# Optimization experiments

Hardware: AMD Instinct MI355X
Metric: run time of the kernel (lower is better)

The kernel has to match this reference:

```python
import jax, jax.numpy as jnp
import numpy as np

HIDDEN = 2048
HEADS = 16
HEAD_DIM = HIDDEN // HEADS
BATCH = 2
SEQ = 2048


def setup_inputs() -> dict:
    key = jax.random.key(0)
    ks = jax.random.split(key, 9)
    s = 0.02
    return {
        "x": jax.random.normal(ks[0], (BATCH, SEQ, HIDDEN), dtype=jnp.float32),
        "wq": jax.random.normal(ks[1], (HIDDEN, HIDDEN), dtype=jnp.float32) * s,
        "bq": jax.random.normal(ks[2], (HIDDEN,), dtype=jnp.float32) * s,
        "wk": jax.random.normal(ks[3], (HIDDEN, HIDDEN), dtype=jnp.float32) * s,
        "bk": jax.random.normal(ks[4], (HIDDEN,), dtype=jnp.float32) * s,
        "wv": jax.random.normal(ks[5], (HIDDEN, HIDDEN), dtype=jnp.float32) * s,
        "bv": jax.random.normal(ks[6], (HIDDEN,), dtype=jnp.float32) * s,
        "wo": jax.random.normal(ks[7], (HIDDEN, HIDDEN), dtype=jnp.float32) * s,
        "bo": jax.random.normal(ks[8], (HIDDEN,), dtype=jnp.float32) * s,
    }


def reference(x, wq, bq, wk, bk, wv, bv, wo, bo):
    B, S, _ = x.shape
    scale = jnp.sqrt(jnp.float32(HEAD_DIM))
    # torch Linear: y = x @ W.T + b
    def proj(w, b):
        return (x @ w.T + b).reshape(B, S, HEADS, HEAD_DIM).transpose(0, 2, 1, 3)
    q = proj(wq, bq)  # [B,H,S,D]
    k = proj(wk, bk)
    v = proj(wv, bv)
    scores = jnp.einsum("bhqd,bhkd->bhqk", q, k) / scale  # [B,H,S,S]
    probs = jax.nn.softmax(scores, axis=-1)
    ctx = jnp.einsum("bhqk,bhkd->bhqd", probs, v)  # [B,H,S,D]
    ctx = ctx.transpose(0, 2, 1, 3).reshape(B, S, HIDDEN)
    return ctx @ wo.T + bo
```

## Files before the change

kernel.cpp:

```cpp
#include <hip/hip_runtime.h>

typedef unsigned short u16;
typedef unsigned int   u32;
typedef float  f32x4   __attribute__((ext_vector_type(4)));
typedef __bf16 bf16x8  __attribute__((ext_vector_type(8)));
typedef u16    u16x8   __attribute__((ext_vector_type(8)));
typedef u16    u16x4   __attribute__((ext_vector_type(4)));
typedef u32    u32x2   __attribute__((ext_vector_type(2)));
typedef u32    u32x4   __attribute__((ext_vector_type(4)));

#define HIDDEN 2048
#define SEQ    2048
#define NHEADS 16
#define HD     128
#define BATCH  2
#define QSTR   4096

typedef const __attribute__((address_space(3))) u16* lptr;

__device__ __forceinline__ u16 f2bf(float f) {
  u32 u = __builtin_bit_cast(u32, f);
  u += 0x7FFFu + ((u >> 16) & 1u);
  return (u16)(u >> 16);
}
__device__ __forceinline__ u32 pk2(float a, float b) {
  __bf16 x = (__bf16)a, y = (__bf16)b;
  return (u32)__builtin_bit_cast(u16, x) | ((u32)__builtin_bit_cast(u16, y) << 16);
}
__device__ __forceinline__ bf16x8 ld_frag(const u16* p) {
  return __builtin_bit_cast(bf16x8, *(const u32x4*)p);
}
__device__ __forceinline__ void gload_lds16(const u16* g, u16* l) {
  __builtin_amdgcn_global_load_lds((const __attribute__((address_space(1))) u32*)g,
                                   (__attribute__((address_space(3))) u32*)l, 16, 0, 0);
}

#define DSR(dst, base, lit) \
  asm volatile("ds_read_b128 %0, %1 offset:" lit : "=v"(dst) : "v"(base))

#define MFMA16(d, a, b) d = __builtin_amdgcn_mfma_f32_16x16x32_bf16(a, b, d, 0, 0, 0)

__global__ __launch_bounds__(256) void cvt_kernel(const float* __restrict__ src,
                                                  u16* __restrict__ dst, int n4) {
  int stride = gridDim.x * blockDim.x;
  for (int i = blockIdx.x * blockDim.x + threadIdx.x; i < n4; i += stride) {
    f32x4 v = ((const f32x4*)src)[i];
    u16x4 o;
    o[0] = f2bf(v[0]); o[1] = f2bf(v[1]); o[2] = f2bf(v[2]); o[3] = f2bf(v[3]);
    *(u16x4*)(dst + (size_t)i * 4) = o;
  }
}

__global__ __launch_bounds__(256) void cvt4_kernel(
    const float* __restrict__ s0, const float* __restrict__ s1,
    const float* __restrict__ s2, const float* __restrict__ s3,
    u16* __restrict__ o0, u16* __restrict__ o1,
    u16* __restrict__ o2, u16* __restrict__ o3, int n4) {
  const float* src = (blockIdx.y == 0) ? s0 : (blockIdx.y == 1) ? s1 : (blockIdx.y == 2) ? s2 : s3;
  u16* dst = (blockIdx.y == 0) ? o0 : (blockIdx.y == 1) ? o1 : (blockIdx.y == 2) ? o2 : o3;
  int stride = gridDim.x * blockDim.x;
  for (int i = blockIdx.x * blockDim.x + threadIdx.x; i < n4; i += stride) {
    f32x4 v = ((const f32x4*)src)[i];
    u16x4 o;
    o[0] = f2bf(v[0]); o[1] = f2bf(v[1]); o[2] = f2bf(v[2]); o[3] = f2bf(v[3]);
    *(u16x4*)(dst + (size_t)i * 4) = o;
  }
}

__global__ __launch_bounds__(512, 2) void gemm_qkv(
    const u16* __restrict__ A, const u16* __restrict__ Bt,
    const float* __restrict__ bq, const float* __restrict__ bk,
    const float* __restrict__ bv,
    u16* __restrict__ qk, u16* __restrict__ vtb, float qscale)
{
  __shared__ __attribute__((aligned(16))) u16 As[2][16384];
  __shared__ __attribute__((aligned(16))) u16 Bs[2][12288];

  const int tid  = threadIdx.x;
  const int lane = tid & 63;
  const int wave = tid >> 6;
  const int l15  = lane & 15;
  const int g    = lane >> 4;
  const int wm   = wave >> 2;
  const int wn   = wave & 3;

  const int id  = blockIdx.x;
  const int xcd = id & 7;
  const int c   = id >> 3;
  const int tileN = (xcd * 4 + (c >> 4)) * 192;
  const int tileM = (c & 15) << 8;

  const int srow = tid >> 3;
  const int gch8 = ((tid & 7) ^ (srow & 7)) * 8;
  const u16* agp = A  + (size_t)(tileM + srow) * HIDDEN + gch8;
  const u16* bgp = Bt + (size_t)(tileN + srow) * HIDDEN + gch8;
  u16* asp = (u16*)&As[0][0] + tid * 8;
  u16* bsp = (u16*)&Bs[0][0] + tid * 8;

  auto stage = [&](int buf, int ko) {
    u16* ad = asp + buf * 16384;
    u16* bd = bsp + buf * 12288;
#pragma unroll
    for (int r = 0; r < 4; ++r)
      gload_lds16(agp + (size_t)r * 64 * HIDDEN + ko, ad + r * 4096);
#pragma unroll
    for (int r = 0; r < 3; ++r)
      gload_lds16(bgp + (size_t)r * 64 * HIDDEN + ko, bd + r * 4096);
  };

  const int sw = l15 & 7;
  const int c0 = (g ^ sw) * 8;
  const int c1 = ((g ^ sw) ^ 4) * 8;
  lptr aT = (lptr)&As[0][0] + (size_t)(wm * 128 + l15) * 64;
  lptr bT = (lptr)&Bs[0][0] + (size_t)(wn * 48 + l15) * 64;

  f32x4 acc[8][3] = {};
  bf16x8 Xa[8], Xb[3], Ya[8], Yb[3];

#define ISSUE_SET(Sa, Sb, ab, bb)      \
  DSR(Sa[0], ab, "0");                 \
  DSR(Sa[1], ab, "2048");              \
  DSR(Sa[2], ab, "4096");              \
  DSR(Sa[3], ab, "6144");              \
  DSR(Sa[4], ab, "8192");              \
  DSR(Sa[5], ab, "10240");             \
  DSR(Sa[6], ab, "12288");             \
  DSR(Sa[7], ab, "14336");             \
  DSR(Sb[0], bb, "0");                 \
  DSR(Sb[1], bb, "2048");              \
  DSR(Sb[2], bb, "4096");

#define MFMA24(Sa, Sb)                                                                    \
  _Pragma("unroll")                                                                       \
  for (int mf = 0; mf < 8; ++mf) {                                                        \
    _Pragma("unroll")                                                                     \
    for (int nf = 0; nf < 3; ++nf)                                                        \
      acc[mf][nf] = __builtin_amdgcn_mfma_f32_16x16x32_bf16(Sa[mf], Sb[nf], acc[mf][nf], 0, 0, 0); \
  }

  stage(0, 0);
  stage(1, 64);
  asm volatile("s_waitcnt vmcnt(7)" ::: "memory");
  __builtin_amdgcn_s_barrier();
  __builtin_amdgcn_sched_barrier(0);
  {
    lptr ab = aT + c0;
    lptr bb = bT + c0;
    ISSUE_SET(Xa, Xb, ab, bb)
  }

#pragma unroll 2
  for (int t = 0; t < 32; ++t) {
    const int cur = t & 1;
    lptr aC = aT + cur * 16384;
    lptr bC = bT + cur * 12288;
    {
      lptr ab = aC + c1;
      lptr bb = bC + c1;
      ISSUE_SET(Ya, Yb, ab, bb)
    }
    asm volatile("s_waitcnt lgkmcnt(11)" ::: "memory");
    __builtin_amdgcn_sched_barrier(0);
    __builtin_amdgcn_s_setprio(1);
    MFMA24(Xa, Xb)
    __builtin_amdgcn_s_setprio(0);
    asm volatile("s_waitcnt lgkmcnt(0)" ::: "memory");
    __builtin_amdgcn_sched_barrier(0);
    __builtin_amdgcn_s_setprio(1);
    MFMA24(Ya, Yb)
    __builtin_amdgcn_s_setprio(0);
    __builtin_amdgcn_s_barrier();
    __builtin_amdgcn_sched_barrier(0);
    if (t < 30) {
      stage(cur, (t + 2) * 64);
      asm volatile("s_waitcnt vmcnt(7)" ::: "memory");
    } else {
      asm volatile("s_waitcnt vmcnt(0)" ::: "memory");
    }
    __builtin_amdgcn_s_barrier();
    __builtin_amdgcn_sched_barrier(0);
    if (t < 31) {
      lptr ab = aT + (cur ^ 1) * 16384 + c0;
      lptr bb = bT + (cur ^ 1) * 12288 + c0;
      ISSUE_SET(Xa, Xb, ab, bb)
    }
  }

#pragma unroll
  for (int mi = 0; mi < 8; ++mi) {
#pragma unroll
    for (int ni = 0; ni < 3; ++ni) {
      const int gcb = tileN + wn * 48 + ni * 16;
      const int seg = gcb >> 11;
      const int gc  = gcb + l15;
      const float bvv = ((seg == 0) ? bq : (seg == 1) ? bk : bv)[gc & 2047];
      if (seg < 2) {
        const float scl = (seg == 0) ? qscale : 1.f;
#pragma unroll
        for (int j = 0; j < 4; ++j) {
          const int gr = tileM + wm * 128 + mi * 16 + g * 4 + j;
          qk[(size_t)gr * QSTR + gc] = f2bf((acc[mi][ni][j] + bvv) * scl);
        }
      } else {
        const int dglob = gc - 4096;
        const int hh = dglob >> 7, dd = dglob & 127;
        const int srow0 = tileM + wm * 128 + mi * 16 + g * 4;
        const int bb = srow0 >> 11, ss = srow0 & 2047;
        u16x4 o;
#pragma unroll
        for (int j = 0; j < 4; ++j) o[j] = f2bf(acc[mi][ni][j] + bvv);
        *(u16x4*)(vtb + ((size_t)((bb * NHEADS + hh) * HD + dd)) * SEQ + ss) = o;
      }
    }
  }
#undef ISSUE_SET
#undef MFMA24
}

__global__ __launch_bounds__(256, 2) void gemm_bt(
    const u16* __restrict__ A, const u16* __restrict__ Bt,
    const float* __restrict__ bias, float* __restrict__ Cout,
    int M, int N, int K)
{
  __shared__ __attribute__((aligned(16))) u16 As[128 * 32];
  __shared__ __attribute__((aligned(16))) u16 Bs[128 * 32];
  const int tid  = threadIdx.x;
  const int lane = tid & 63;
  const int wave = tid >> 6;

  const int nbx   = N >> 7;
  const int nby   = M >> 7;
  const int id    = blockIdx.x;
  const int xcd   = id & 7;
  const int c     = id >> 3;
  const int cpx   = nbx >> 3;
  const int tileN = (xcd * cpx + c / nby) << 7;
  const int tileM = (c % nby) << 7;

  const int g = lane >> 4, r = lane & 15;

  const int srow = lane >> 2;
  const int scol = (lane & 3) * 8;
  const u16* ag0 = A  + (size_t)(tileM + wave * 16 + srow) * K + scol;
  const u16* ag1 = ag0 + (size_t)64 * K;
  const u16* bg0 = Bt + (size_t)(tileN + wave * 16 + srow) * K + scol;
  const u16* bg1 = bg0 + (size_t)64 * K;
  u16* as0 = &As[wave * 512];
  u16* as1 = &As[(wave + 4) * 512];
  u16* bs0 = &Bs[wave * 512];
  u16* bs1 = &Bs[(wave + 4) * 512];

  const int wm = wave >> 1, wn = wave & 1;
  const u16* afp = &As[(wm * 64 + r) * 32 + g * 8];
  const u16* bfp = &Bs[(wn * 64 + r) * 32 + g * 8];

  f32x4 acc[4][4] = {};

  for (int kt = 0; kt < K; kt += 32) {
    __syncthreads();
    gload_lds16(ag0 + kt, as0);
    gload_lds16(ag1 + kt, as1);
    gload_lds16(bg0 + kt, bs0);
    gload_lds16(bg1 + kt, bs1);
    __syncthreads();
    bf16x8 af[4], bf[4];
#pragma unroll
    for (int mi = 0; mi < 4; mi++) af[mi] = ld_frag(afp + mi * 512);
#pragma unroll
    for (int ni = 0; ni < 4; ni++) bf[ni] = ld_frag(bfp + ni * 512);
#pragma unroll
    for (int mi = 0; mi < 4; mi++)
#pragma unroll
      for (int ni = 0; ni < 4; ni++)
        acc[mi][ni] = __builtin_amdgcn_mfma_f32_16x16x32_bf16(af[mi], bf[ni], acc[mi][ni], 0, 0, 0);
  }

#pragma unroll
  for (int mi = 0; mi < 4; mi++) {
#pragma unroll
    for (int ni = 0; ni < 4; ni++) {
      const int gc = tileN + wn * 64 + ni * 16 + r;
      const float bv = bias[gc];
#pragma unroll
      for (int j = 0; j < 4; j++) {
        const int gr = tileM + wm * 64 + mi * 16 + g * 4 + j;
        Cout[(size_t)gr * N + gc] = acc[mi][ni][j] + bv;
      }
    }
  }
}

__global__ __launch_bounds__(256, 2) void attn_kernel(
    const u16* __restrict__ QKg, const u16* __restrict__ Vtg, u16* __restrict__ Ctx)
{
  __shared__ __attribute__((aligned(16))) u16 Ks[2][64 * 128];
  __shared__ __attribute__((aligned(16))) u16 Vs[2][128 * 64];

  const int tid  = threadIdx.x;
  const int lane = tid & 63;
  const int wave = tid >> 6;
  const int g4   = lane >> 4;
  const int l15  = lane & 15;

  const int wg = ((blockIdx.x & 7) << 6) + (blockIdx.x >> 3);
  const int bh = wg >> 4;
  const int qt = wg & 15;
  const int b  = bh >> 4, h = bh & 15;

  const u16* Qb  = QKg + (size_t)b * SEQ * QSTR + (size_t)h * HD;
  const u16* Kb  = Qb + 2048;
  const u16* Vth = Vtg + (size_t)bh * HD * SEQ;
  u16* Cb = Ctx + (size_t)b * SEQ * HIDDEN + (size_t)h * HD;

  const int qbase = qt * 128 + wave * 32 + l15;

  bf16x8 qf[2][4];
#pragma unroll
  for (int qs = 0; qs < 2; qs++)
#pragma unroll
    for (int dc = 0; dc < 4; dc++)
      qf[qs][dc] = ld_frag(Qb + (size_t)(qbase + qs * 16) * QSTR + dc * 32 + g4 * 8);

  const int kvp0 = (l15 >> 2) * 8 + (l15 & 3);
  const int msw  = (l15 & 3) | (((l15 >> 2) & 1) << 2);
  const int msw3 = msw & 3;
  const int mk   = (l15 >> 2) & 1;
  const int kcol = (g4 ^ msw3) * 8;

  lptr ksb = (lptr)&Ks[0][0];
  lptr kE0 = ksb + (kvp0      ) * 128 + kcol + mk * 32;
  lptr kO0 = ksb + (kvp0      ) * 128 + kcol + (1 ^ mk) * 32;
  lptr kE1 = ksb + (kvp0 +   4) * 128 + kcol + mk * 32;
  lptr kO1 = ksb + (kvp0 +   4) * 128 + kcol + (1 ^ mk) * 32;
  lptr kE2 = ksb + (kvp0 +  32) * 128 + kcol + mk * 32;
  lptr kO2 = ksb + (kvp0 +  32) * 128 + kcol + (1 ^ mk) * 32;
  lptr kE3 = ksb + (kvp0 +  36) * 128 + kcol + mk * 32;
  lptr kO3 = ksb + (kvp0 +  36) * 128 + kcol + (1 ^ mk) * 32;

  lptr vsb = (lptr)&Vs[0][0];
  lptr vB0 = vsb + l15 * 64 + ((0 * 4 + g4) ^ (l15 & 7)) * 8;
  lptr vB1 = vsb + l15 * 64 + ((1 * 4 + g4) ^ (l15 & 7)) * 8;

  const u16* kg[4];
  const u16* vg[4];
  u16* ksd = (u16*)&Ks[0][0] + tid * 8;
  u16* vsd = (u16*)&Vs[0][0] + tid * 8;
#pragma unroll
  for (int i = 0; i < 4; i++) {
    const int idx = tid + i * 256;
    const int kv = idx >> 4, up = idx & 15;
    const int um = up ^ ((kv & 3) | (((kv >> 3) & 1) << 2));
    kg[i] = Kb + (size_t)kv * QSTR + um * 8;
    const int d = idx >> 3, u = idx & 7;
    const int uv = u ^ (d & 7);
    vg[i] = Vth + (size_t)d * SEQ + uv * 8;
  }

  auto stage = [&](int buf, int kv0) {
    u16* kd = ksd + buf * 8192;
    u16* vd = vsd + buf * 8192;
#pragma unroll
    for (int i = 0; i < 4; i++) gload_lds16(kg[i] + (size_t)kv0 * QSTR, kd + i * 2048);
#pragma unroll
    for (int i = 0; i < 4; i++) gload_lds16(vg[i] + kv0, vd + i * 2048);
  };

  f32x4 ctx[2][8] = {};
  float m_run[2] = {-1e30f, -1e30f};
  float l_run[2] = {0.f, 0.f};

  stage(0, 0);

  const int NT = SEQ / 64;
  for (int t = 0; t < NT; t++) {
    const int buf = t & 1;

    if (t + 1 < NT) {
      stage(buf ^ 1, (t + 1) * 64);
      asm volatile("s_waitcnt vmcnt(8)" ::: "memory");
    } else {
      asm volatile("s_waitcnt vmcnt(0)" ::: "memory");
    }
    __builtin_amdgcn_s_barrier();
    __builtin_amdgcn_sched_barrier(0);

    bf16x8 kf[4][4];
    {
      const int bo = buf * 8192;
      lptr e0 = kE0 + bo, o0 = kO0 + bo, e1 = kE1 + bo, o1 = kO1 + bo;
      lptr e2 = kE2 + bo, o2 = kO2 + bo, e3 = kE3 + bo, o3 = kO3 + bo;
      DSR(kf[0][0], e0, "0"); DSR(kf[0][1], o0, "0"); DSR(kf[0][2], e0, "128"); DSR(kf[0][3], o0, "128");
      DSR(kf[1][0], e1, "0"); DSR(kf[1][1], o1, "0"); DSR(kf[1][2], e1, "128"); DSR(kf[1][3], o1, "128");
      DSR(kf[2][0], e2, "0"); DSR(kf[2][1], o2, "0"); DSR(kf[2][2], e2, "128"); DSR(kf[2][3], o2, "128");
      DSR(kf[3][0], e3, "0"); DSR(kf[3][1], o3, "0"); DSR(kf[3][2], e3, "128"); DSR(kf[3][3], o3, "128");
    }
    f32x4 s[2][4] = {};
    asm volatile("s_waitcnt lgkmcnt(8)" ::: "memory");
    __builtin_amdgcn_sched_barrier(0);
    __builtin_amdgcn_s_setprio(1);
#pragma unroll
    for (int ni = 0; ni < 2; ni++)
#pragma unroll
      for (int dc = 0; dc < 4; dc++) {
        MFMA16(s[0][ni], kf[ni][dc], qf[0][dc]);
        MFMA16(s[1][ni], kf[ni][dc], qf[1][dc]);
      }
    __builtin_amdgcn_sched_barrier(0);
    asm volatile("s_waitcnt lgkmcnt(0)" ::: "memory");
    __builtin_amdgcn_sched_barrier(0);
#pragma unroll
    for (int ni = 2; ni < 4; ni++)
#pragma unroll
      for (int dc = 0; dc < 4; dc++) {
        MFMA16(s[0][ni], kf[ni][dc], qf[0][dc]);
        MFMA16(s[1][ni], kf[ni][dc], qf[1][dc]);
      }
    __builtin_amdgcn_s_setprio(0);
    __builtin_amdgcn_sched_barrier(0);

    float pmax[2];
#pragma unroll
    for (int qs = 0; qs < 2; qs++) {
      float m0 = fmaxf(fmaxf(s[qs][0][0], s[qs][0][1]), fmaxf(s[qs][0][2], s[qs][0][3]));
      float m1 = fmaxf(fmaxf(s[qs][1][0], s[qs][1][1]), fmaxf(s[qs][1][2], s[qs][1][3]));
      float m2 = fmaxf(fmaxf(s[qs][2][0], s[qs][2][1]), fmaxf(s[qs][2][2], s[qs][2][3]));
      float m3 = fmaxf(fmaxf(s[qs][3][0], s[qs][3][1]), fmaxf(s[qs][3][2], s[qs][3][3]));
      pmax[qs] = fmaxf(fmaxf(m0, m1), fmaxf(m2, m3));
      pmax[qs] = fmaxf(pmax[qs], __shfl_xor(pmax[qs], 16));
      pmax[qs] = fmaxf(pmax[qs], __shfl_xor(pmax[qs], 32));
    }
    const bool ok0 = (pmax[0] <= m_run[0] + 8.f);
    const bool ok1 = (pmax[1] <= m_run[1] + 8.f);
    if (!__all(ok0 && ok1)) {
#pragma unroll
      for (int qs = 0; qs < 2; qs++) {
        const float mn = fmaxf(m_run[qs], pmax[qs]);
        const float corr = exp2f(m_run[qs] - mn);
        m_run[qs] = mn;
        l_run[qs] *= corr;
#pragma unroll
        for (int dt = 0; dt < 8; dt++)
#pragma unroll
          for (int j = 0; j < 4; j++) ctx[qs][dt][j] *= corr;
      }
    }
    bf16x8 pfrag[2][2];
#pragma unroll
    for (int qs = 0; qs < 2; qs++) {
      float ps = 0.f;
#pragma unroll
      for (int ni = 0; ni < 4; ni++)
#pragma unroll
        for (int j = 0; j < 4; j++) {
          const float p = exp2f(s[qs][ni][j] - m_run[qs]);
          s[qs][ni][j] = p;
          ps += p;
        }
      ps += __shfl_xor(ps, 16);
      ps += __shfl_xor(ps, 32);
      l_run[qs] += ps;
#pragma unroll
      for (int hh = 0; hh < 2; hh++) {
        u32x4 pw;
        pw[0] = pk2(s[qs][2 * hh][0], s[qs][2 * hh][1]);
        pw[1] = pk2(s[qs][2 * hh][2], s[qs][2 * hh][3]);
        pw[2] = pk2(s[qs][2 * hh + 1][0], s[qs][2 * hh + 1][1]);
        pw[3] = pk2(s[qs][2 * hh + 1][2], s[qs][2 * hh + 1][3]);
        pfrag[qs][hh] = __builtin_bit_cast(bf16x8, pw);
      }
    }
    __builtin_amdgcn_sched_barrier(0);

    bf16x8 vf[2][8];
    {
      lptr v0 = vB0 + buf * 8192;
      lptr v1 = vB1 + buf * 8192;
      DSR(vf[0][0], v0, "0");     DSR(vf[0][1], v0, "2048");
      DSR(vf[0][2], v0, "4096");  DSR(vf[0][3], v0, "6144");
      DSR(vf[0][4], v0, "8192");  DSR(vf[0][5], v0, "10240");
      DSR(vf[0][6], v0, "12288"); DSR(vf[0][7], v0, "14336");
      DSR(vf[1][0], v1, "0");     DSR(vf[1][1], v1, "2048");
      DSR(vf[1][2], v1, "4096");  DSR(vf[1][3], v1, "6144");
      DSR(vf[1][4], v1, "8192");  DSR(vf[1][5], v1, "10240");
      DSR(vf[1][6], v1, "12288"); DSR(vf[1][7], v1, "14336");
    }
    asm volatile("s_waitcnt lgkmcnt(8)" ::: "memory");
    __builtin_amdgcn_sched_barrier(0);
    __builtin_amdgcn_s_setprio(1);
#pragma unroll
    for (int dt = 0; dt < 8; dt++) {
      MFMA16(ctx[0][dt], vf[0][dt], pfrag[0][0]);
      MFMA16(ctx[1][dt], vf[0][dt], pfrag[1][0]);
    }
    __builtin_amdgcn_sched_barrier(0);
    asm volatile("s_waitcnt lgkmcnt(0)" ::: "memory");
    __builtin_amdgcn_sched_barrier(0);
#pragma unroll
    for (int dt = 0; dt < 8; dt++) {
      MFMA16(ctx[0][dt], vf[1][dt], pfrag[0][1]);
      MFMA16(ctx[1][dt], vf[1][dt], pfrag[1][1]);
    }
    __builtin_amdgcn_s_setprio(0);
    __builtin_amdgcn_sched_barrier(0);

    __builtin_amdgcn_s_barrier();
    __builtin_amdgcn_sched_barrier(0);
  }

#pragma unroll
  for (int qs = 0; qs < 2; qs++) {
    const float linv = 1.f / l_run[qs];
    u16* crow = Cb + (size_t)(qbase + qs * 16) * HIDDEN;
#pragma unroll
    for (int dt = 0; dt < 8; dt++) {
      u16x4 o;
#pragma unroll
      for (int j = 0; j < 4; j++) o[j] = f2bf(ctx[qs][dt][j] * linv);
      *(u16x4*)&crow[dt * 16 + g4 * 4] = o;
    }
  }
}

extern "C" void kernel_launch(void* const* d_in, const int* in_sizes, int n_in,
                              void* d_out, int out_size, void* d_ws, size_t ws_size,
                              hipStream_t stream) {
  (void)in_sizes; (void)n_in; (void)out_size; (void)ws_size;
  const float* x  = (const float*)d_in[0];
  const float* wq = (const float*)d_in[1];
  const float* bq = (const float*)d_in[2];
  const float* wk = (const float*)d_in[3];
  const float* bk = (const float*)d_in[4];
  const float* wv = (const float*)d_in[5];
  const float* bv = (const float*)d_in[6];
  const float* wo = (const float*)d_in[7];
  const float* bo = (const float*)d_in[8];

  const size_t NX = (size_t)BATCH * SEQ * HIDDEN;
  const size_t NW = (size_t)HIDDEN * HIDDEN;
  u16* xb   = (u16*)d_ws;
  u16* wqb  = xb  + NX;
  u16* wkb  = wqb + NW;
  u16* wvb  = wkb + NW;
  u16* wob  = wvb + NW;
  u16* qk   = wob + NW;
  u16* vtb  = qk  + 2 * NX;
  u16* ctxb = xb;

  cvt_kernel<<<2048, 256, 0, stream>>>(x, xb, (int)(NX / 4));
  cvt4_kernel<<<dim3(512, 4), 256, 0, stream>>>(wq, wk, wv, wo, wqb, wkb, wvb, wob, (int)(NW / 4));

  const float qscale = 0.12751744174240807f;
  gemm_qkv<<<512, 512, 0, stream>>>(xb, wqb, bq, bk, bv, qk, vtb, qscale);

  attn_kernel<<<512, 256, 0, stream>>>(qk, vtb, ctxb);

  gemm_bt<<<512, 256, 0, stream>>>(ctxb, wob, bo, (float*)d_out, BATCH * SEQ, HIDDEN, HIDDEN);
}
```

Before: 277.8 us.

## Pipeline output GEMM, move QKV staging earlier, defer softmax row-sum reduction

Replaces the simple output-projection GEMM with a double-buffered, swizzled-LDS kernel using 512 threads, 256x128 tiles, and an interleaved ds_read/MFMA schedule. In the QKV GEMM the next-tile global-to-LDS staging is issued before the second MFMA half, so loads overlap more compute. In attention the per-iteration cross-lane shuffle reduction of the row sum moves to a single reduction at the end, which is valid because the rescale factor is uniform across the row. Together these target memory stalls and shuffle overhead, at the cost of more LDS use and lower occupancy in the new GEMM.

```diff
diff --git a/kernel.cpp b/kernel.cpp
--- a/kernel.cpp
+++ b/kernel.cpp
@@ -166,13 +166,15 @@
     __builtin_amdgcn_s_setprio(0);
     asm volatile("s_waitcnt lgkmcnt(0)" ::: "memory");
     __builtin_amdgcn_sched_barrier(0);
+    __builtin_amdgcn_s_barrier();
+    __builtin_amdgcn_sched_barrier(0);
+    if (t < 30) stage(cur, (t + 2) * 64);
+    __builtin_amdgcn_sched_barrier(0);
     __builtin_amdgcn_s_setprio(1);
     MFMA24(Ya, Yb)
     __builtin_amdgcn_s_setprio(0);
-    __builtin_amdgcn_s_barrier();
     __builtin_amdgcn_sched_barrier(0);
     if (t < 30) {
-      stage(cur, (t + 2) * 64);
       asm volatile("s_waitcnt vmcnt(7)" ::: "memory");
     } else {
       asm volatile("s_waitcnt vmcnt(0)" ::: "memory");
@@ -217,74 +219,126 @@
 #undef MFMA24
 }
 
-__global__ __launch_bounds__(256, 2) void gemm_bt(
+__global__ __launch_bounds__(512, 2) void gemm_o(
     const u16* __restrict__ A, const u16* __restrict__ Bt,
-    const float* __restrict__ bias, float* __restrict__ Cout,
-    int M, int N, int K)
+    const float* __restrict__ bias, float* __restrict__ Cout)
 {
-  __shared__ __attribute__((aligned(16))) u16 As[128 * 32];
-  __shared__ __attribute__((aligned(16))) u16 Bs[128 * 32];
+  __shared__ __attribute__((aligned(16))) u16 As[2][16384];
+  __shared__ __attribute__((aligned(16))) u16 Bs[2][8192];
+
   const int tid  = threadIdx.x;
   const int lane = tid & 63;
   const int wave = tid >> 6;
-
-  const int nbx   = N >> 7;
-  const int nby   = M >> 7;
-  const int id    = blockIdx.x;
-  const int xcd   = id & 7;
-  const int c     = id >> 3;
-  const int cpx   = nbx >> 3;
-  const int tileN = (xcd * cpx + c / nby) << 7;
-  const int tileM = (c % nby) << 7;
-
-  const int g = lane >> 4, r = lane & 15;
-
-  const int srow = lane >> 2;
-  const int scol = (lane & 3) * 8;
-  const u16* ag0 = A  + (size_t)(tileM + wave * 16 + srow) * K + scol;
-  const u16* ag1 = ag0 + (size_t)64 * K;
-  const u16* bg0 = Bt + (size_t)(tileN + wave * 16 + srow) * K + scol;
-  const u16* bg1 = bg0 + (size_t)64 * K;
-  u16* as0 = &As[wave * 512];
-  u16* as1 = &As[(wave + 4) * 512];
-  u16* bs0 = &Bs[wave * 512];
-  u16* bs1 = &Bs[(wave + 4) * 512];
-
-  const int wm = wave >> 1, wn = wave & 1;
-  const u16* afp = &As[(wm * 64 + r) * 32 + g * 8];
-  const u16* bfp = &Bs[(wn * 64 + r) * 32 + g * 8];
+  const int l15  = lane & 15;
+  const int g    = lane >> 4;
+  const int wm   = wave >> 1;
+  const int wn   = wave & 1;
+
+  const int id  = blockIdx.x;
+  const int xcd = id & 7;
+  const int c   = id >> 3;
+  const int tileN = (xcd * 2 + (c >> 4)) << 7;
+  const int tileM = (c & 15) << 8;
+
+  const int sr   = tid >> 3;
+  const int sgc  = ((tid & 7) ^ (sr & 7)) * 8;
+  const u16* agp = A  + (size_t)(tileM + sr) * HIDDEN + sgc;
+  const u16* bgp = Bt + (size_t)(tileN + sr) * HIDDEN + sgc;
+  u16* asp = (u16*)&As[0][0] + tid * 8;
+  u16* bsp = (u16*)&Bs[0][0] + tid * 8;
+
+  auto stage = [&](int buf, int ko) {
+    u16* ad = asp + buf * 16384;
+    u16* bd = bsp + buf * 8192;
+#pragma unroll
+    for (int r = 0; r < 4; ++r)
+      gload_lds16(agp + (size_t)r * 64 * HIDDEN + ko, ad + r * 4096);
+#pragma unroll
+    for (int r = 0; r < 2; ++r)
+      gload_lds16(bgp + (size_t)r * 64 * HIDDEN + ko, bd + r * 4096);
+  };
+
+  const int sw = l15 & 7;
+  const int c0 = (g ^ sw) * 8;
+  const int c1 = ((g ^ sw) ^ 4) * 8;
+  lptr aT = (lptr)&As[0][0] + (size_t)(wm * 64 + l15) * 64;
+  lptr bT = (lptr)&Bs[0][0] + (size_t)(wn * 64 + l15) * 64;
 
   f32x4 acc[4][4] = {};
-
-  for (int kt = 0; kt < K; kt += 32) {
-    __syncthreads();
-    gload_lds16(ag0 + kt, as0);
-    gload_lds16(ag1 + kt, as1);
-    gload_lds16(bg0 + kt, bs0);
-    gload_lds16(bg1 + kt, bs1);
-    __syncthreads();
-    bf16x8 af[4], bf[4];
-#pragma unroll
-    for (int mi = 0; mi < 4; mi++) af[mi] = ld_frag(afp + mi * 512);
-#pragma unroll
-    for (int ni = 0; ni < 4; ni++) bf[ni] = ld_frag(bfp + ni * 512);
-#pragma unroll
-    for (int mi = 0; mi < 4; mi++)
-#pragma unroll
-      for (int ni = 0; ni < 4; ni++)
-        acc[mi][ni] = __builtin_amdgcn_mfma_f32_16x16x32_bf16(af[mi], bf[ni], acc[mi][ni], 0, 0, 0);
-  }
-
-#pragma unroll
-  for (int mi = 0; mi < 4; mi++) {
-#pragma unroll
-    for (int ni = 0; ni < 4; ni++) {
-      const int gc = tileN + wn * 64 + ni * 16 + r;
+  bf16x8 Xa[4], Xb[4], Ya[4], Yb[4];
+
+#define ISSUE8O(Sa, Sb, ab, bb) \
+  DSR(Sa[0], ab, "0"); DSR(Sa[1], ab, "2048"); DSR(Sa[2], ab, "4096"); DSR(Sa[3], ab, "6144"); \
+  DSR(Sb[0], bb, "0"); DSR(Sb[1], bb, "2048"); DSR(Sb[2], bb, "4096"); DSR(Sb[3], bb, "6144");
+
+#define MFMA16O(Sa, Sb)                                                                   \
+  _Pragma("unroll")                                                                       \
+  for (int mf = 0; mf < 4; ++mf) {                                                        \
+    _Pragma("unroll")                                                                     \
+    for (int nf = 0; nf < 4; ++nf)                                                        \
+      acc[mf][nf] = __builtin_amdgcn_mfma_f32_16x16x32_bf16(Sa[mf], Sb[nf], acc[mf][nf], 0, 0, 0); \
+  }
+
+  stage(0, 0);
+  stage(1, 64);
+  asm volatile("s_waitcnt vmcnt(6)" ::: "memory");
+  __builtin_amdgcn_s_barrier();
+  __builtin_amdgcn_sched_barrier(0);
+  {
+    lptr ab = aT + c0;
+    lptr bb = bT + c0;
+    ISSUE8O(Xa, Xb, ab, bb)
+  }
+
+#pragma unroll 2
+  for (int t = 0; t < 32; ++t) {
+    const int cur = t & 1;
+    {
+      lptr ab = aT + cur * 16384 + c1;
+      lptr bb = bT + cur * 8192 + c1;
+      ISSUE8O(Ya, Yb, ab, bb)
+    }
+    asm volatile("s_waitcnt lgkmcnt(8)" ::: "memory");
+    __builtin_amdgcn_sched_barrier(0);
+    __builtin_amdgcn_s_setprio(1);
+    MFMA16O(Xa, Xb)
+    __builtin_amdgcn_s_setprio(0);
+    asm volatile("s_waitcnt lgkmcnt(0)" ::: "memory");
+    __builtin_amdgcn_sched_barrier(0);
+    __builtin_amdgcn_s_barrier();
+    __builtin_amdgcn_sched_barrier(0);
+    if (t < 30) stage(cur, (t + 2) * 64);
+    __builtin_amdgcn_sched_barrier(0);
+    __builtin_amdgcn_s_setprio(1);
+    MFMA16O(Ya, Yb)
+    __builtin_amdgcn_s_setprio(0);
+    __builtin_amdgcn_sched_barrier(0);
+    if (t < 30) {
+      asm volatile("s_waitcnt vmcnt(6)" ::: "memory");
+    } else {
+      asm volatile("s_waitcnt vmcnt(0)" ::: "memory");
+    }
+    __builtin_amdgcn_s_barrier();
+    __builtin_amdgcn_sched_barrier(0);
+    if (t < 31) {
+      lptr ab = aT + (cur ^ 1) * 16384 + c0;
+      lptr bb = bT + (cur ^ 1) * 8192 + c0;
+      ISSUE8O(Xa, Xb, ab, bb)
+    }
+  }
+#undef ISSUE8O
+#undef MFMA16O
+
+#pragma unroll
+  for (int mf = 0; mf < 4; ++mf) {
+#pragma unroll
+    for (int nf = 0; nf < 4; ++nf) {
+      const int gc = tileN + wn * 64 + nf * 16 + l15;
       const float bv = bias[gc];
 #pragma unroll
-      for (int j = 0; j < 4; j++) {
-        const int gr = tileM + wm * 64 + mi * 16 + g * 4 + j;
-        Cout[(size_t)gr * N + gc] = acc[mi][ni][j] + bv;
+      for (int j = 0; j < 4; ++j) {
+        const int gr = tileM + wm * 64 + mf * 16 + g * 4 + j;
+        Cout[(size_t)gr * HIDDEN + gc] = acc[mf][nf][j] + bv;
       }
     }
   }
@@ -456,8 +510,6 @@
           s[qs][ni][j] = p;
           ps += p;
         }
-      ps += __shfl_xor(ps, 16);
-      ps += __shfl_xor(ps, 32);
       l_run[qs] += ps;
 #pragma unroll
       for (int hh = 0; hh < 2; hh++) {
@@ -509,7 +561,10 @@
 
 #pragma unroll
   for (int qs = 0; qs < 2; qs++) {
-    const float linv = 1.f / l_run[qs];
+    float lt = l_run[qs];
+    lt += __shfl_xor(lt, 16);
+    lt += __shfl_xor(lt, 32);
+    const float linv = 1.f / lt;
     u16* crow = Cb + (size_t)(qbase + qs * 16) * HIDDEN;
 #pragma unroll
     for (int dt = 0; dt < 8; dt++) {
@@ -554,5 +609,5 @@
 
   attn_kernel<<<512, 256, 0, stream>>>(qk, vtb, ctxb);
 
-  gemm_bt<<<512, 256, 0, stream>>>(ctxb, wob, bo, (float*)d_out, BATCH * SEQ, HIDDEN, HIDDEN);
-}
+  gemm_o<<<256, 512, 0, stream>>>(ctxb, wob, bo, (float*)d_out);
+}
```

Result: faster. 250.1 us (-9.9%).
